# Optimization experiments

Hardware: AMD Instinct MI355X
Metric: run time of the kernel (lower is better)

Reference implementation:

```python
import jax, jax.numpy as jnp
import numpy as np

N, D, BS, M, DC, H, DH, L, E = 16384, 512, 16, 256, 512, 8, 64, 4, 262144
EPS = 1e-5


def _ln(x, w, b):
    mu = jnp.mean(x, -1, keepdims=True)
    var = jnp.var(x, -1, keepdims=True)
    return (x - mu) * jax.lax.rsqrt(var + EPS) * w + b


def _gcn(x, src, dst, W, b, n):
    deg = jax.ops.segment_sum(jnp.ones_like(src, dtype=x.dtype), dst, num_segments=n)
    dinv = jnp.where(deg > 0, deg ** -0.5, 0.0)
    norm = dinv[src] * dinv[dst]  # [E+N]
    h = x @ W
    out = jax.ops.segment_sum(h[src] * norm[:, None], dst, num_segments=n)
    return out + b


def _attn(xf, cond, Wq, Wk, Wv, Wo):
    n, d = xf.shape
    xb = xf.reshape(BS, n // BS, d)                    # stack(chunk(x, bs))
    q = (xb @ Wq).reshape(BS, -1, H, DH)
    k = (cond @ Wk).reshape(BS, -1, H, DH)
    v = (cond @ Wv).reshape(BS, -1, H, DH)
    att = jnp.einsum('bnhd,bmhd->bhnm', q, k) * (DH ** -0.5)
    w = jax.nn.softmax(att, axis=-1)
    o = jnp.einsum('bhnm,bmhd->bnhd', w, v).reshape(BS, -1, H * DH)
    return (o @ Wo).reshape(n, d)


def setup_inputs() -> dict:
    key = jax.random.key(0)
    ks = jax.random.split(key, 24)
    s = lambda fi, fo: (2.0 / (fi + fo)) ** 0.5
    inp = {
        'x': jax.random.normal(ks[0], (N, D), jnp.float32),
        'edge_index': jax.random.randint(ks[1], (2, E), 0, N, jnp.int64),
        'cond': jax.random.normal(ks[2], (BS, M, DC), jnp.float32),
        'bn_w': jnp.ones((D,), jnp.float32),
        'bn_b': jnp.zeros((D,), jnp.float32),
        'gcn_in_w': jax.random.normal(ks[3], (D, D), jnp.float32) * s(D, D),
        'gcn_in_b': jnp.zeros((D,), jnp.float32),
        'gcn_out_w': jax.random.normal(ks[4], (D, D), jnp.float32) * s(D, D),
        'gcn_out_b': jnp.zeros((D,), jnp.float32),
        'Wq': jax.random.normal(ks[5], (L, D, H * DH), jnp.float32) * s(D, H * DH),
        'Wk': jax.random.normal(ks[6], (L, DC, H * DH), jnp.float32) * s(DC, H * DH),
        'Wv': jax.random.normal(ks[7], (L, DC, H * DH), jnp.float32) * s(DC, H * DH),
        'Wo': jax.random.normal(ks[8], (L, H * DH, D), jnp.float32) * s(H * DH, D),
        'ln2_w': jnp.ones((L, D), jnp.float32),
        'ln2_b': jnp.zeros((L, D), jnp.float32),
        'ln3_w': jnp.ones((L, D), jnp.float32),
        'ln3_b': jnp.zeros((L, D), jnp.float32),
        'geglu_w': jax.random.normal(ks[9], (L, D, 8 * D), jnp.float32) * s(D, 8 * D),
        'geglu_b': jnp.zeros((L, 8 * D), jnp.float32),
        'ffo_w': jax.random.normal(ks[10], (L, 4 * D, D), jnp.float32) * s(4 * D, D),
        'ffo_b': jnp.zeros((L, D), jnp.float32),
    }
    return inp


def reference(x, edge_index, cond, bn_w, bn_b, gcn_in_w, gcn_in_b, gcn_out_w,
              gcn_out_b, Wq, Wk, Wv, Wo, ln2_w, ln2_b, ln3_w, ln3_b,
              geglu_w, geglu_b, ffo_w, ffo_b):
    n = x.shape[0]
    loops = jnp.arange(n)
    src = jnp.concatenate([edge_index[0], loops])
    dst = jnp.concatenate([edge_index[1], loops])

    x_in = x
    # BatchNorm1d (training mode: batch stats, biased var)
    mu = jnp.mean(x, 0)
    var = jnp.var(x, 0)
    h = (x - mu) * jax.lax.rsqrt(var + EPS) * bn_w + bn_b

    h = _gcn(h, src, dst, gcn_in_w, gcn_in_b, n)

    for i in range(L):
        a = _attn(_ln(h, ln2_w[i], ln2_b[i]), cond, Wq[i], Wk[i], Wv[i], Wo[i])
        h = h + a
        u = _ln(h, ln3_w[i], ln3_b[i]) @ geglu_w[i] + geglu_b[i]
        val, gate = jnp.split(u, 2, axis=-1)
        f = val * jax.nn.gelu(gate, approximate=False)
        h = h + f @ ffo_w[i] + ffo_b[i]

    h = _gcn(h, src, dst, gcn_out_w, gcn_out_b, n)
    return h + x_in
```

## Files before the change

kernel.cpp:

```cpp
#include <hip/hip_runtime.h>
#include <math.h>
#include <stdio.h>

#define N_NODES 16384
#define DIM     512
#define BSZ     16
#define SEQ     1024
#define MCTX    256
#define NHEAD   8
#define DHEAD   64
#define NLAYER  4
#define NEDGE   262144
#define DFF     2048
#define DG      4096
#define LNEPS   1e-5f

typedef unsigned short u16;
typedef __attribute__((ext_vector_type(8))) __bf16 bf16x8;
typedef __attribute__((ext_vector_type(4))) float f32x4;
typedef __attribute__((ext_vector_type(4))) unsigned short u16x4;
typedef __attribute__((ext_vector_type(8))) unsigned short u16x8;

__device__ __forceinline__ u16 f2b(float f) {
    unsigned u = __float_as_uint(f);
    unsigned r = (u + 0x7fff + ((u >> 16) & 1)) >> 16;
    return (u16)r;
}
__device__ __forceinline__ float b2f(u16 h) {
    return __uint_as_float((unsigned)h << 16);
}
__device__ __forceinline__ float gelu_exact(float x) {
    return 0.5f * x * (1.0f + erff(x * 0.70710678118654752f));
}
__device__ __forceinline__ void gload16(const void* g, void* l) {
    __builtin_amdgcn_global_load_lds(
        (const __attribute__((address_space(1))) unsigned int*)g,
        (__attribute__((address_space(3))) unsigned int*)l, 16, 0, 0);
}

__device__ __forceinline__ int2 xcd_map() {
    int gx = gridDim.x, gy = gridDim.y;
    int nwg = gx * gy;
    int id = blockIdx.y * gx + blockIdx.x;
    int q = nwg >> 3, r = nwg & 7;
    int xcd = id & 7, idx = id >> 3;
    int nid = (xcd < r ? xcd * (q + 1) : r * (q + 1) + (xcd - r) * q) + idx;
    int2 o; o.x = nid % gx; o.y = nid / gx; return o;
}

__global__ __launch_bounds__(512, 2) void bgemm256_geglu(
    const u16* __restrict__ A, long lda,
    const u16* __restrict__ Bt, long ldb,
    const float* __restrict__ bias,
    u16* __restrict__ Cb, int K)
{
    __shared__ u16 lds[65536];

    const int t = threadIdx.x;
    const int w = t >> 6, lane = t & 63;
    const int fr = lane & 15, fq = lane >> 4;
    int2 sw = xcd_map();
    const int row0 = sw.y * 256;
    const int col0 = sw.x * 256;
    const int wm0 = (w >> 2) * 128, wn0 = (w & 3) * 64;
    const int sl = (lane & 7) ^ ((lane >> 3) & 7);

    f32x4 acc[8][4];
#pragma unroll
    for (int mf = 0; mf < 8; ++mf)
#pragma unroll
        for (int nf = 0; nf < 4; ++nf) acc[mf][nf] = (f32x4){0.f, 0.f, 0.f, 0.f};

    auto stageA = [&](int kt_, int P, int bb) {
        const int k0 = kt_ << 6;
#pragma unroll
        for (int rd = 0; rd < 2; ++rd) {
            int rbase = rd * 128 + P * 64 + w * 8;
            int r = rbase + (lane >> 3);
            gload16(A + (size_t)(row0 + r) * lda + k0 + sl * 8,
                    (char*)(lds + bb * 16384) + rbase * 128);
        }
    };
    auto stageB = [&](int kt_, int Q, int bb) {
        const int k0 = kt_ << 6;
#pragma unroll
        for (int rd = 0; rd < 2; ++rd) {
            int jb = rd * 64 + w * 8;
            int nbase = ((jb >> 5) << 6) + Q * 32 + (jb & 31);
            int n = nbase + (lane >> 3);
            gload16(Bt + (size_t)(col0 + n) * ldb + k0 + sl * 8,
                    (char*)(lds + 32768 + bb * 16384) + nbase * 128);
        }
    };

#define PHASE(MH, NH, STAGE_STMT, WC) do {                                    \
    const u16* Ab_ = lds + b * 16384;                                         \
    const u16* Bb_ = lds + 32768 + b * 16384;                                 \
    bf16x8 av[4][2], bv[2][2];                                                \
    _Pragma("unroll")                                                         \
    for (int mi = 0; mi < 4; ++mi) {                                          \
        int r = wm0 + MH * 64 + mi * 16 + fr;                                 \
        _Pragma("unroll")                                                     \
        for (int ks = 0; ks < 2; ++ks)                                        \
            av[mi][ks] = *(const bf16x8*)&Ab_[r * 64 + (((ks*4+fq) ^ (fr&7)) * 8)]; \
    }                                                                         \
    _Pragma("unroll")                                                         \
    for (int ni = 0; ni < 2; ++ni) {                                          \
        int n = wn0 + NH * 32 + ni * 16 + fr;                                 \
        _Pragma("unroll")                                                     \
        for (int ks = 0; ks < 2; ++ks)                                        \
            bv[ni][ks] = *(const bf16x8*)&Bb_[n * 64 + (((ks*4+fq) ^ (fr&7)) * 8)]; \
    }                                                                         \
    STAGE_STMT;                                                               \
    __builtin_amdgcn_s_barrier();                                             \
    asm volatile("s_waitcnt lgkmcnt(0)" ::: "memory");                        \
    __builtin_amdgcn_s_setprio(1);                                            \
    _Pragma("unroll")                                                         \
    for (int mi = 0; mi < 4; ++mi)                                            \
        _Pragma("unroll")                                                     \
        for (int ni = 0; ni < 2; ++ni)                                        \
            _Pragma("unroll")                                                 \
            for (int ks = 0; ks < 2; ++ks)                                    \
                acc[MH*4+mi][NH*2+ni] = __builtin_amdgcn_mfma_f32_16x16x32_bf16( \
                    av[mi][ks], bv[ni][ks], acc[MH*4+mi][NH*2+ni], 0, 0, 0);  \
    __builtin_amdgcn_s_setprio(0);                                            \
    { int wc_ = (WC);                                                         \
      if (wc_ == 4)      asm volatile("s_waitcnt vmcnt(4)" ::: "memory");     \
      else if (wc_ == 0) asm volatile("s_waitcnt vmcnt(0)" ::: "memory"); }   \
    __builtin_amdgcn_s_barrier();                                             \
} while (0)

    stageA(0, 0, 0); stageB(0, 0, 0); stageA(0, 1, 0); stageB(0, 1, 0);
    stageA(1, 0, 1); stageB(1, 0, 1);
    asm volatile("s_waitcnt vmcnt(4)" ::: "memory");
    __builtin_amdgcn_s_barrier();

    const int NT = K >> 6;
    for (int kt = 0; kt < NT; ++kt) {
        const int b = kt & 1;
        const bool s1 = (kt + 1 < NT), s2 = (kt + 2 < NT);
        PHASE(0, 0, if (s1) stageA(kt + 1, 1, b ^ 1), -1);
        PHASE(0, 1, if (s1) stageB(kt + 1, 1, b ^ 1), -1);
        PHASE(1, 0, if (s2) stageA(kt + 2, 0, b), -1);
        PHASE(1, 1, if (s2) stageB(kt + 2, 0, b), s2 ? 4 : (s1 ? 0 : -1));
    }
#undef PHASE

    const int nbase = (col0 + wn0) >> 1;
    float bval[2], bgat[2];
#pragma unroll
    for (int P = 0; P < 2; ++P) {
        int n = nbase + P * 16 + fr;
        bval[P] = bias[n];
        bgat[P] = bias[DFF + n];
    }
#pragma unroll
    for (int mf = 0; mf < 8; ++mf) {
        const int rb = row0 + wm0 + mf * 16 + fq * 4;
#pragma unroll
        for (int P = 0; P < 2; ++P) {
            const int n = nbase + P * 16 + fr;
#pragma unroll
            for (int j = 0; j < 4; ++j) {
                float v = acc[mf][2 * P][j] + bval[P];
                float g = acc[mf][2 * P + 1][j] + bgat[P];
                Cb[(size_t)(rb + j) * DFF + n] = f2b(v * gelu_exact(g));
            }
        }
    }
}

template<int EPI>
__global__ __launch_bounds__(256) void bgemm(
    const u16* __restrict__ A, long lda,
    const u16* __restrict__ Bt, long ldb,
    const float* __restrict__ bias,
    const float* __restrict__ resid, long ldr,
    const float* __restrict__ rowscale,
    void* __restrict__ Cv, long ldc, int K, int nlo,
    long aHi, long aLo, long bHi, long bLo, long cHi, long cLo)
{
    __shared__ u16 lds[32768];

    const int t = threadIdx.x;
    const int z = blockIdx.z;
    const int zhi = z / nlo, zlo = z % nlo;
    const u16* Ag = A + (size_t)zhi * aHi + (size_t)zlo * aLo;
    const u16* Bg = Bt + (size_t)zhi * bHi + (size_t)zlo * bLo;
    const long coff = (long)zhi * cHi + (long)zlo * cLo;

    int2 sw = xcd_map();
    const int row0 = sw.y * 128;
    const int col0 = sw.x * 128;
    const int wave = t >> 6, lane = t & 63;
    const int wm0 = (wave >> 1) * 64, wn0 = (wave & 1) * 64;
    const int fr = lane & 15, fq = lane >> 4;
    const int ldsWave = (t & 192) * 16;
    const int rS = t >> 3;
    const int slotP = t & 7;

    f32x4 acc[4][4];
#pragma unroll
    for (int mi = 0; mi < 4; ++mi)
#pragma unroll
        for (int ni = 0; ni < 4; ++ni) acc[mi][ni] = (f32x4){0.f, 0.f, 0.f, 0.f};

    auto stage = [&](int buf, int k0) {
        u16* Ad = lds + buf * 8192;
        u16* Bd = lds + 16384 + buf * 8192;
#pragma unroll
        for (int i = 0; i < 4; ++i) {
            int r = i * 32 + rS;
            int s2 = slotP ^ (r & 7);
            gload16(Ag + (size_t)(row0 + r) * lda + k0 + s2 * 8,
                    (char*)Ad + i * 4096 + ldsWave);
        }
#pragma unroll
        for (int i = 0; i < 4; ++i) {
            int r = i * 32 + rS;
            int s2 = slotP ^ (r & 7);
            gload16(Bg + (size_t)(col0 + r) * ldb + k0 + s2 * 8,
                    (char*)Bd + i * 4096 + ldsWave);
        }
    };
    auto compute = [&](int buf) {
        const u16* Ac = lds + buf * 8192;
        const u16* Bc = lds + 16384 + buf * 8192;
#pragma unroll
        for (int ks = 0; ks < 2; ++ks) {
            const int ksl = ks * 4 + fq;
            bf16x8 av[4], bv[4];
#pragma unroll
            for (int mi = 0; mi < 4; ++mi) {
                int r = wm0 + mi * 16 + fr;
                av[mi] = *(const bf16x8*)&Ac[r * 64 + ((ksl ^ (r & 7)) * 8)];
            }
#pragma unroll
            for (int ni = 0; ni < 4; ++ni) {
                int r = wn0 + ni * 16 + fr;
                bv[ni] = *(const bf16x8*)&Bc[r * 64 + ((ksl ^ (r & 7)) * 8)];
            }
#pragma unroll
            for (int mi = 0; mi < 4; ++mi)
#pragma unroll
                for (int ni = 0; ni < 4; ++ni)
                    acc[mi][ni] = __builtin_amdgcn_mfma_f32_16x16x32_bf16(
                        av[mi], bv[ni], acc[mi][ni], 0, 0, 0);
        }
    };

    int cur = 0;
    stage(0, 0);
    __syncthreads();
    for (int k0 = 64; k0 < K; k0 += 64) {
        stage(cur ^ 1, k0);
        compute(cur);
        __syncthreads();
        cur ^= 1;
    }
    compute(cur);

    if (EPI == 3) {
        __syncthreads();
        u16* Tw = lds + wave * 4608;
#pragma unroll
        for (int mi = 0; mi < 4; ++mi)
#pragma unroll
            for (int ni = 0; ni < 4; ++ni)
#pragma unroll
                for (int j = 0; j < 4; ++j)
                    Tw[(ni * 16 + fr) * 72 + mi * 16 + fq * 4 + j] =
                        f2b(acc[mi][ni][j]);
        const int r0w = row0 + wm0;
        const int b = r0w >> 8, m0w = r0w & 255;
        const int cc0 = col0 + wn0, hh = cc0 >> 6;
        u16* dst = (u16*)Cv + ((size_t)(b * 8 + hh) * 64) * 256 + m0w;
#pragma unroll
        for (int it = 0; it < 8; ++it) {
            int dl = it * 8 + (lane >> 3);
            int ml = (lane & 7) * 8;
            u16x8 v = *(const u16x8*)&Tw[dl * 72 + ml];
            *(u16x8*)&dst[(size_t)dl * 256 + ml] = v;
        }
        return;
    }

    float* Cf = (float*)Cv;
    u16* Cb = (u16*)Cv;
#pragma unroll
    for (int mi = 0; mi < 4; ++mi) {
        const int rb = row0 + wm0 + mi * 16 + fq * 4;
#pragma unroll
        for (int ni = 0; ni < 4; ++ni) {
            const int cc = col0 + wn0 + ni * 16 + fr;
            f32x4 v = acc[mi][ni];
            float bval = 0.f;
            if ((EPI == 1 || EPI == 2) && bias) bval = bias[cc];
#pragma unroll
            for (int j = 0; j < 4; ++j) {
                const long r = rb + j;
                float o = v[j] + bval;
                if (EPI == 1) {
                    Cb[coff + r * ldc + cc] = f2b(o);
                } else if (EPI == 2) {
                    Cf[coff + r * ldc + cc] = o + resid[r * ldr + cc];
                } else if (EPI == 4) {
                    Cb[coff + r * ldc + cc] = f2b(o * rowscale[r]);
                }
            }
        }
    }
}

__global__ __launch_bounds__(256) void transposeW(const float* __restrict__ src,
                                                  u16* __restrict__ dst,
                                                  int K, int N,
                                                  long srcZ, long dstZ, int permN)
{
    __shared__ float tile[64][65];
    const int t = threadIdx.x;
    const int n0 = blockIdx.x * 64, k0 = blockIdx.y * 64;
    const float* s = src + (size_t)blockIdx.z * srcZ;
    u16* d = dst + (size_t)blockIdx.z * dstZ;
#pragma unroll
    for (int i = 0; i < 16; ++i) {
        int idx = i * 256 + t;
        int rr = idx >> 6, cc = idx & 63;
        tile[rr][cc] = s[(size_t)(k0 + rr) * N + n0 + cc];
    }
    __syncthreads();
#pragma unroll
    for (int i = 0; i < 16; ++i) {
        int idx = i * 256 + t;
        int rr = idx >> 6, cc = idx & 63;
        int n = n0 + rr;
        int p = n;
        if (permN) {
            p = (n < permN) ? (((n >> 4) << 5) + (n & 15))
                            : ((((n - permN) >> 4) << 5) + 16 + ((n - permN) & 15));
        }
        d[(size_t)p * K + k0 + cc] = f2b(tile[cc][rr]);
    }
}

__global__ __launch_bounds__(256) void conv_f2b(const float* __restrict__ in,
                                                u16* __restrict__ out)
{
    size_t i = (size_t)blockIdx.x * 256 + threadIdx.x;
    float4 v = ((const float4*)in)[i];
    u16x4 o;
    o[0] = f2b(v.x); o[1] = f2b(v.y); o[2] = f2b(v.z); o[3] = f2b(v.w);
    ((u16x4*)out)[i] = o;
}

__global__ __launch_bounds__(512) void bn_colstats(const float* __restrict__ x,
                                                   float* __restrict__ cs,
                                                   float* __restrict__ cq)
{
    int c = threadIdx.x;
    int r0 = blockIdx.x * 128;
    float s = 0.f, q = 0.f;
    for (int r = 0; r < 128; ++r) {
        float v = x[(size_t)(r0 + r) * DIM + c];
        s += v; q += v * v;
    }
    atomicAdd(&cs[c], s);
    atomicAdd(&cq[c], q);
}

__global__ void bn_finalize(const float* __restrict__ cs, const float* __restrict__ cq,
                            const float* __restrict__ bw, const float* __restrict__ bb,
                            float* __restrict__ scale, float* __restrict__ shift)
{
    int c = threadIdx.x;
    float m   = cs[c] * (1.f / N_NODES);
    float var = cq[c] * (1.f / N_NODES) - m * m;
    float rs  = rsqrtf(var + LNEPS);
    float sc  = rs * bw[c];
    scale[c] = sc;
    shift[c] = bb[c] - m * sc;
}

__global__ __launch_bounds__(256) void bn_apply_b(const float* __restrict__ x,
                                                  const float* __restrict__ scale,
                                                  const float* __restrict__ shift,
                                                  u16* __restrict__ out)
{
    size_t idx = (size_t)blockIdx.x * 256 + threadIdx.x;
    int c4 = (int)(idx & 127);
    float4 v  = ((const float4*)x)[idx];
    float4 sc = ((const float4*)scale)[c4];
    float4 sh = ((const float4*)shift)[c4];
    u16x4 o;
    o[0] = f2b(v.x * sc.x + sh.x); o[1] = f2b(v.y * sc.y + sh.y);
    o[2] = f2b(v.z * sc.z + sh.z); o[3] = f2b(v.w * sc.w + sh.w);
    ((u16x4*)out)[idx] = o;
}

__global__ __launch_bounds__(256) void layernorm_b(const float* __restrict__ in,
                                                   const float* __restrict__ w,
                                                   const float* __restrict__ bsh,
                                                   u16* __restrict__ out)
{
    int lane = threadIdx.x & 63, wv = threadIdx.x >> 6;
    size_t row = (size_t)blockIdx.x * 4 + wv;
    const float* p = in + row * DIM + lane * 8;
    float4 v0 = *(const float4*)p;
    float4 v1 = *(const float4*)(p + 4);
    float s = v0.x + v0.y + v0.z + v0.w + v1.x + v1.y + v1.z + v1.w;
    float q = v0.x * v0.x + v0.y * v0.y + v0.z * v0.z + v0.w * v0.w +
              v1.x * v1.x + v1.y * v1.y + v1.z * v1.z + v1.w * v1.w;
    for (int m = 1; m < 64; m <<= 1) {
        s += __shfl_xor(s, m, 64);
        q += __shfl_xor(q, m, 64);
    }
    float mean = s * (1.f / DIM);
    float rs = rsqrtf(q * (1.f / DIM) - mean * mean + LNEPS);
    float4 w0 = *(const float4*)(w + lane * 8),   w1 = *(const float4*)(w + lane * 8 + 4);
    float4 b0 = *(const float4*)(bsh + lane * 8), b1 = *(const float4*)(bsh + lane * 8 + 4);
    u16x8 o;
    o[0] = f2b((v0.x - mean) * rs * w0.x + b0.x);
    o[1] = f2b((v0.y - mean) * rs * w0.y + b0.y);
    o[2] = f2b((v0.z - mean) * rs * w0.z + b0.z);
    o[3] = f2b((v0.w - mean) * rs * w0.w + b0.w);
    o[4] = f2b((v1.x - mean) * rs * w1.x + b1.x);
    o[5] = f2b((v1.y - mean) * rs * w1.y + b1.y);
    o[6] = f2b((v1.z - mean) * rs * w1.z + b1.z);
    o[7] = f2b((v1.w - mean) * rs * w1.w + b1.w);
    *(u16x8*)(out + row * DIM + lane * 8) = o;
}

__global__ __launch_bounds__(256) void fused_attn(
    const u16* __restrict__ Q,
    const u16* __restrict__ Kp,
    const u16* __restrict__ Vt,
    u16* __restrict__ O)
{
    __shared__ u16 Ks[256 * 64];
    __shared__ u16 Vs[64 * 256];
    __shared__ u16 Ps[4][16 * 256];

    const int t = threadIdx.x;
    const int wave = t >> 6, lane = t & 63;
    const int fr = lane & 15, fq = lane >> 4;
    const int qc = blockIdx.x, h = blockIdx.y, b = blockIdx.z;
    const int ldsW = (t & 192) * 16;

#pragma unroll
    for (int i = 0; i < 8; ++i) {
        int idx = i * 256 + t;
        int m = idx >> 3, s = idx & 7;
        gload16(Kp + (size_t)(b * MCTX + m) * 512 + h * 64 + ((s ^ (m & 7)) * 8),
                (char*)Ks + i * 4096 + ldsW);
    }
#pragma unroll
    for (int i = 0; i < 8; ++i) {
        int idx = i * 256 + t;
        int d = idx >> 5, s = idx & 31;
        gload16(Vt + (size_t)((b * 8 + h) * 64 + d) * 256 + ((s ^ (d & 7)) * 8),
                (char*)Vs + i * 4096 + ldsW);
    }
    __syncthreads();

    u16* Pw = Ps[wave];
    for (int it = 0; it < 4; ++it) {
        const int q0 = qc * 256 + it * 64 + wave * 16;
        bf16x8 aq[2];
#pragma unroll
        for (int ks = 0; ks < 2; ++ks)
            aq[ks] = *(const bf16x8*)&Q[(size_t)(b * SEQ + q0 + fr) * 512 +
                                        h * 64 + ks * 32 + fq * 8];
        f32x4 accS[16];
#pragma unroll
        for (int ni = 0; ni < 16; ++ni) accS[ni] = (f32x4){0.f, 0.f, 0.f, 0.f};
#pragma unroll
        for (int ni = 0; ni < 16; ++ni) {
            int m = ni * 16 + fr;
#pragma unroll
            for (int ks = 0; ks < 2; ++ks) {
                bf16x8 bv = *(const bf16x8*)&Ks[m * 64 + (((ks * 4 + fq) ^ (m & 7)) * 8)];
                accS[ni] = __builtin_amdgcn_mfma_f32_16x16x32_bf16(
                    aq[ks], bv, accS[ni], 0, 0, 0);
            }
        }
        const float cs = 0.125f;
#pragma unroll
        for (int j = 0; j < 4; ++j) {
            float m0 = accS[0][j];
#pragma unroll
            for (int ni = 1; ni < 16; ++ni) m0 = fmaxf(m0, accS[ni][j]);
            m0 = fmaxf(m0, __shfl_xor(m0, 1, 64));
            m0 = fmaxf(m0, __shfl_xor(m0, 2, 64));
            m0 = fmaxf(m0, __shfl_xor(m0, 4, 64));
            m0 = fmaxf(m0, __shfl_xor(m0, 8, 64));
            float s0 = 0.f;
#pragma unroll
            for (int ni = 0; ni < 16; ++ni) {
                float p = __expf((accS[ni][j] - m0) * cs);
                accS[ni][j] = p;
                s0 += p;
            }
            s0 += __shfl_xor(s0, 1, 64);
            s0 += __shfl_xor(s0, 2, 64);
            s0 += __shfl_xor(s0, 4, 64);
            s0 += __shfl_xor(s0, 8, 64);
            float inv = 1.f / s0;
#pragma unroll
            for (int ni = 0; ni < 16; ++ni) {
                int cc = ni * 16 + fr;
                int rr = fq * 4 + j;
                Pw[rr * 256 + (((cc >> 3) ^ (rr & 7)) * 8) + (cc & 7)] =
                    f2b(accS[ni][j] * inv);
            }
        }
        bf16x8 ap[8];
#pragma unroll
        for (int ks = 0; ks < 8; ++ks)
            ap[ks] = *(const bf16x8*)&Pw[fr * 256 + (((ks * 4 + fq) ^ (fr & 7)) * 8)];
        f32x4 accO[4];
#pragma unroll
        for (int ni = 0; ni < 4; ++ni) accO[ni] = (f32x4){0.f, 0.f, 0.f, 0.f};
#pragma unroll
        for (int ni = 0; ni < 4; ++ni) {
            int d = ni * 16 + fr;
#pragma unroll
            for (int ks = 0; ks < 8; ++ks) {
                bf16x8 bv = *(const bf16x8*)&Vs[d * 256 + (((ks * 4 + fq) ^ (d & 7)) * 8)];
                accO[ni] = __builtin_amdgcn_mfma_f32_16x16x32_bf16(
                    ap[ks], bv, accO[ni], 0, 0, 0);
            }
        }
#pragma unroll
        for (int ni = 0; ni < 4; ++ni)
#pragma unroll
            for (int j = 0; j < 4; ++j)
                O[(size_t)(b * SEQ + q0 + fq * 4 + j) * 512 + h * 64 + ni * 16 + fr] =
                    f2b(accO[ni][j]);
    }
}

__global__ void detect_i64(const int* __restrict__ e, int* __restrict__ flag)
{
    int idx = blockIdx.x * blockDim.x + threadIdx.x;
    if (e[2 * idx + 1] != 0) flag[0] = 1;
}

__global__ void deg_count(const int* __restrict__ eb, const int* __restrict__ flag,
                          int* __restrict__ deg)
{
    int e = blockIdx.x * blockDim.x + threadIdx.x;
    int d;
    if (flag[0]) d = eb[NEDGE + e];
    else         d = (int)((const long long*)eb)[NEDGE + e];
    atomicAdd(&deg[d], 1);
}

__global__ void dinv_k(const int* __restrict__ deg, float* __restrict__ dinv)
{
    int i = blockIdx.x * blockDim.x + threadIdx.x;
    dinv[i] = rsqrtf((float)(deg[i] + 1));
}

__global__ __launch_bounds__(1024) void scan_deg(const int* __restrict__ deg,
                                                 int* __restrict__ off)
{
    __shared__ int sums[1024];
    int t = threadIdx.x;
    int base = t * 16;
    int v[16]; int s = 0;
#pragma unroll
    for (int i = 0; i < 16; ++i) { v[i] = deg[base + i]; s += v[i]; }
    sums[t] = s;
    __syncthreads();
    for (int ofs = 1; ofs < 1024; ofs <<= 1) {
        int x = (t >= ofs) ? sums[t - ofs] : 0;
        __syncthreads();
        sums[t] += x;
        __syncthreads();
    }
    int run = (t == 0) ? 0 : sums[t - 1];
#pragma unroll
    for (int i = 0; i < 16; ++i) { off[base + i] = run; run += v[i]; }
    if (t == 1023) off[N_NODES] = run;
}

__global__ void fill_k(const int* __restrict__ eb, const int* __restrict__ flag,
                       const int* __restrict__ off, int* __restrict__ cursor,
                       int* __restrict__ csr)
{
    int e = blockIdx.x * blockDim.x + threadIdx.x;
    int s, d;
    if (flag[0]) { s = eb[e]; d = eb[NEDGE + e]; }
    else {
        const long long* p = (const long long*)eb;
        s = (int)p[e]; d = (int)p[NEDGE + e];
    }
    int pos = atomicAdd(&cursor[d], 1);
    csr[off[d] + pos] = s;
}

__global__ __launch_bounds__(256) void gcn_gather(
    const u16* __restrict__ h2, const int* __restrict__ csr,
    const int* __restrict__ off, const float* __restrict__ dinv,
    const float* __restrict__ bias, const float* __restrict__ addx,
    float* __restrict__ out)
{
    int lane = threadIdx.x & 63, wv = threadIdx.x >> 6;
    int d = blockIdx.x * 4 + wv;
    float acc[8];
#pragma unroll
    for (int j = 0; j < 8; ++j) acc[j] = 0.f;
    int e0 = off[d], e1 = off[d + 1];
    float dd = dinv[d];
    int sidx = (e0 < e1) ? csr[e0] : d;
    u16x8 v = *(const u16x8*)&h2[(size_t)sidx * DIM + lane * 8];
    for (int e = e0; e < e1; ++e) {
        int snext = (e + 1 < e1) ? csr[e + 1] : d;
        u16x8 vn = *(const u16x8*)&h2[(size_t)snext * DIM + lane * 8];
#pragma unroll
        for (int j = 0; j < 8; ++j) acc[j] += b2f(v[j]);
        v = vn;
    }
#pragma unroll
    for (int j = 0; j < 8; ++j) acc[j] = (acc[j] + b2f(v[j])) * dd;
    float o[8];
#pragma unroll
    for (int j = 0; j < 8; ++j) {
        o[j] = acc[j] + bias[lane * 8 + j];
        if (addx) o[j] += addx[(size_t)d * DIM + lane * 8 + j];
    }
    float* op = out + (size_t)d * DIM + lane * 8;
    *(float4*)op = make_float4(o[0], o[1], o[2], o[3]);
    *(float4*)(op + 4) = make_float4(o[4], o[5], o[6], o[7]);
}

extern "C" void kernel_launch(void* const* d_in, const int* in_sizes, int n_in,
                              void* d_out, int out_size, void* d_ws, size_t ws_size,
                              hipStream_t stream)
{
    const float* x         = (const float*)d_in[0];
    const int*   edges     = (const int*)d_in[1];
    const float* cond      = (const float*)d_in[2];
    const float* bn_w      = (const float*)d_in[3];
    const float* bn_b      = (const float*)d_in[4];
    const float* gcn_in_w  = (const float*)d_in[5];
    const float* gcn_in_b  = (const float*)d_in[6];
    const float* gcn_out_w = (const float*)d_in[7];
    const float* gcn_out_b = (const float*)d_in[8];
    const float* Wq  = (const float*)d_in[9];
    const float* Wk  = (const float*)d_in[10];
    const float* Wv  = (const float*)d_in[11];
    const float* Wo  = (const float*)d_in[12];
    const float* ln2w = (const float*)d_in[13];
    const float* ln2b = (const float*)d_in[14];
    const float* ln3w = (const float*)d_in[15];
    const float* ln3b = (const float*)d_in[16];
    const float* ggw = (const float*)d_in[17];
    const float* ggb = (const float*)d_in[18];
    const float* fow = (const float*)d_in[19];
    const float* fob = (const float*)d_in[20];
    float* outp = (float*)d_out;

    char* wsb = (char*)d_ws;
    size_t wsoff = 0;
    auto alloc = [&](size_t bytes) -> void* {
        void* p = wsb + wsoff;
        wsoff = (wsoff + bytes + 255) & ~(size_t)255;
        return p;
    };
    u16*   wT    = (u16*)  alloc((size_t)17301504 * 2);
    u16*   condb = (u16*)  alloc((size_t)4096 * 512 * 2);
    float* h     = (float*)alloc((size_t)N_NODES * DIM * 4);
    u16*   t0b   = (u16*)  alloc((size_t)N_NODES * DIM * 2);
    u16*   qb    = (u16*)  alloc((size_t)N_NODES * DIM * 2);
    u16*   ob    = (u16*)  alloc((size_t)N_NODES * DIM * 2);
    u16*   kb    = (u16*)  alloc((size_t)4096 * 512 * 2);
    u16*   Vt    = (u16*)  alloc((size_t)BSZ * NHEAD * DHEAD * MCTX * 2);
    char*  zbase  = wsb + wsoff;
    float* colsum = (float*)alloc(DIM * 4);
    float* colsq  = (float*)alloc(DIM * 4);
    int*   deg    = (int*)  alloc(N_NODES * 4);
    int*   cursor = (int*)  alloc(N_NODES * 4);
    int*   eflag  = (int*)  alloc(256);
    size_t zbytes = (size_t)((wsb + wsoff) - zbase);
    float* bscale = (float*)alloc(DIM * 4);
    float* bshift = (float*)alloc(DIM * 4);
    float* dinv   = (float*)alloc(N_NODES * 4);
    int*   csr_off= (int*)  alloc((N_NODES + 16) * 4);
    int*   csr_src= (int*)  alloc((size_t)NEDGE * 4);

    int nch = 0;
    for (int c = 1; c <= 16; c *= 2) {
        size_t need = ((size_t)N_NODES / c) * DFF * 2;
        if (wsoff + need <= ws_size) { nch = c; break; }
    }
    if (nch == 0) { fprintf(stderr, "ws too small (%zu)\n", ws_size); return; }
    u16* Abuf = (u16*)(wsb + wsoff);

    hipMemsetAsync(zbase, 0, zbytes, stream);

    u16* gcnInT  = wT;
    u16* gcnOutT = gcnInT + 262144;
    u16* WqT = gcnOutT + 262144;
    u16* WkT = WqT + 4 * 262144;
    u16* WvT = WkT + 4 * 262144;
    u16* WoT = WvT + 4 * 262144;
    u16* ggT = WoT + 4 * 262144;
    u16* foT = ggT + 4 * 2097152;
    transposeW<<<dim3(8, 8, 1), 256, 0, stream>>>(gcn_in_w,  gcnInT, 512, 512, 0, 0, 0);
    transposeW<<<dim3(8, 8, 1), 256, 0, stream>>>(gcn_out_w, gcnOutT, 512, 512, 0, 0, 0);
    transposeW<<<dim3(8, 8, 4), 256, 0, stream>>>(Wq, WqT, 512, 512, 262144, 262144, 0);
    transposeW<<<dim3(8, 8, 4), 256, 0, stream>>>(Wk, WkT, 512, 512, 262144, 262144, 0);
    transposeW<<<dim3(8, 8, 4), 256, 0, stream>>>(Wv, WvT, 512, 512, 262144, 262144, 0);
    transposeW<<<dim3(8, 8, 4), 256, 0, stream>>>(Wo, WoT, 512, 512, 262144, 262144, 0);
    transposeW<<<dim3(64, 8, 4), 256, 0, stream>>>(ggw, ggT, 512, DG, 2097152, 2097152, DFF);
    transposeW<<<dim3(8, 32, 4), 256, 0, stream>>>(fow, foT, DFF, 512, 1048576, 1048576, 0);
    conv_f2b<<<2048, 256, 0, stream>>>(cond, condb);

    bn_colstats<<<128, 512, 0, stream>>>(x, colsum, colsq);
    bn_finalize<<<1, 512, 0, stream>>>(colsum, colsq, bn_w, bn_b, bscale, bshift);
    bn_apply_b<<<(N_NODES * DIM / 4) / 256, 256, 0, stream>>>(x, bscale, bshift, t0b);

    detect_i64<<<NEDGE / 256, 256, 0, stream>>>(edges, eflag);
    deg_count<<<NEDGE / 256, 256, 0, stream>>>(edges, eflag, deg);
    dinv_k<<<N_NODES / 256, 256, 0, stream>>>(deg, dinv);
    scan_deg<<<1, 1024, 0, stream>>>(deg, csr_off);
    fill_k<<<NEDGE / 256, 256, 0, stream>>>(edges, eflag, csr_off, cursor, csr_src);

    bgemm<4><<<dim3(4, 128, 1), 256, 0, stream>>>(
        t0b, 512, gcnInT, 512, nullptr, nullptr, 0, dinv, qb, 512, 512, 1,
        0, 0, 0, 0, 0, 0);
    gcn_gather<<<N_NODES / 4, 256, 0, stream>>>(qb, csr_src, csr_off, dinv,
                                                gcn_in_b, nullptr, h);

    const int ffrows = N_NODES / nch;
    for (int i = 0; i < NLAYER; ++i) {
        const u16* WqTi = WqT + (size_t)i * 262144;
        const u16* WkTi = WkT + (size_t)i * 262144;
        const u16* WvTi = WvT + (size_t)i * 262144;
        const u16* WoTi = WoT + (size_t)i * 262144;
        const u16* ggTi = ggT + (size_t)i * 2097152;
        const u16* foTi = foT + (size_t)i * 1048576;

        layernorm_b<<<N_NODES / 4, 256, 0, stream>>>(h, ln2w + i * DIM, ln2b + i * DIM, t0b);
        bgemm<1><<<dim3(4, 128, 1), 256, 0, stream>>>(
            t0b, 512, WqTi, 512, nullptr, nullptr, 0, nullptr, qb, 512, 512, 1,
            0, 0, 0, 0, 0, 0);
        bgemm<1><<<dim3(4, 32, 1), 256, 0, stream>>>(
            condb, 512, WkTi, 512, nullptr, nullptr, 0, nullptr, kb, 512, 512, 1,
            0, 0, 0, 0, 0, 0);
        bgemm<3><<<dim3(4, 32, 1), 256, 0, stream>>>(
            condb, 512, WvTi, 512, nullptr, nullptr, 0, nullptr, Vt, 0, 512, 1,
            0, 0, 0, 0, 0, 0);
        fused_attn<<<dim3(4, 8, 16), 256, 0, stream>>>(qb, kb, Vt, ob);
        bgemm<2><<<dim3(4, 128, 1), 256, 0, stream>>>(
            ob, 512, WoTi, 512, nullptr, h, 512, nullptr, h, 512, 512, 1,
            0, 0, 0, 0, 0, 0);

        layernorm_b<<<N_NODES / 4, 256, 0, stream>>>(h, ln3w + i * DIM, ln3b + i * DIM, t0b);
        for (int c = 0; c < nch; ++c) {
            const u16* ac = t0b + (size_t)c * ffrows * 512;
            float* hc = h + (size_t)c * ffrows * 512;
            bgemm256_geglu<<<dim3(DG / 256, ffrows / 256), 512, 0, stream>>>(
                ac, 512, ggTi, 512, ggb + (size_t)i * DG, Abuf, 512);
            bgemm<2><<<dim3(4, ffrows / 128, 1), 256, 0, stream>>>(
                Abuf, 2048, foTi, 2048, fob + (size_t)i * DIM, hc, 512, nullptr,
                hc, 512, 2048, 1, 0, 0, 0, 0, 0, 0);
        }
    }

    conv_f2b<<<8192, 256, 0, stream>>>(h, t0b);
    bgemm<4><<<dim3(4, 128, 1), 256, 0, stream>>>(
        t0b, 512, gcnOutT, 512, nullptr, nullptr, 0, dinv, qb, 512, 512, 1,
        0, 0, 0, 0, 0, 0);
    gcn_gather<<<N_NODES / 4, 256, 0, stream>>>(qb, csr_src, csr_off, dinv,
                                                gcn_out_b, x, outp);
}
```

Measured before the change: 1.323 ms.

## Reorder GEGLU MFMA phases for register reuse, tanh GELU, batch K/V projections

Three changes. The GEGLU GEMM inner loop now reuses A and B fragments across its four phases in a snake order, so the last phase does no LDS reads. The exact erf GELU is swapped for a tanh approximation built on exp. The per-layer K and V projections of cond are hoisted out of the layer loop into two batched launches over all layers, which adds buffers that hold K/V for every layer. The tanh GELU changes numerics away from the reference's exact GELU, which risks going past the accuracy tolerance.

```diff
diff --git a/kernel.cpp b/kernel.cpp
--- a/kernel.cpp
+++ b/kernel.cpp
@@ -32,6 +32,12 @@
 __device__ __forceinline__ float gelu_exact(float x) {
     return 0.5f * x * (1.0f + erff(x * 0.70710678118654752f));
 }
+__device__ __forceinline__ float gelu_fast(float x) {
+    float u = x * (0.7978845608f + 0.0356774081f * x * x);
+    float e = __expf(2.f * u);
+    float t = 1.f - 2.f / (e + 1.f);
+    return 0.5f * x * (1.f + t);
+}
 __device__ __forceinline__ void gload16(const void* g, void* l) {
     __builtin_amdgcn_global_load_lds(
         (const __attribute__((address_space(1))) unsigned int*)g,
@@ -93,42 +99,31 @@
         }
     };
 
-#define PHASE(MH, NH, STAGE_STMT, WC) do {                                    \
-    const u16* Ab_ = lds + b * 16384;                                         \
-    const u16* Bb_ = lds + 32768 + b * 16384;                                 \
-    bf16x8 av[4][2], bv[2][2];                                                \
-    _Pragma("unroll")                                                         \
-    for (int mi = 0; mi < 4; ++mi) {                                          \
-        int r = wm0 + MH * 64 + mi * 16 + fr;                                 \
-        _Pragma("unroll")                                                     \
-        for (int ks = 0; ks < 2; ++ks)                                        \
-            av[mi][ks] = *(const bf16x8*)&Ab_[r * 64 + (((ks*4+fq) ^ (fr&7)) * 8)]; \
-    }                                                                         \
-    _Pragma("unroll")                                                         \
-    for (int ni = 0; ni < 2; ++ni) {                                          \
-        int n = wn0 + NH * 32 + ni * 16 + fr;                                 \
-        _Pragma("unroll")                                                     \
-        for (int ks = 0; ks < 2; ++ks)                                        \
-            bv[ni][ks] = *(const bf16x8*)&Bb_[n * 64 + (((ks*4+fq) ^ (fr&7)) * 8)]; \
-    }                                                                         \
-    STAGE_STMT;                                                               \
-    __builtin_amdgcn_s_barrier();                                             \
-    asm volatile("s_waitcnt lgkmcnt(0)" ::: "memory");                        \
-    __builtin_amdgcn_s_setprio(1);                                            \
-    _Pragma("unroll")                                                         \
-    for (int mi = 0; mi < 4; ++mi)                                            \
-        _Pragma("unroll")                                                     \
-        for (int ni = 0; ni < 2; ++ni)                                        \
-            _Pragma("unroll")                                                 \
-            for (int ks = 0; ks < 2; ++ks)                                    \
-                acc[MH*4+mi][NH*2+ni] = __builtin_amdgcn_mfma_f32_16x16x32_bf16( \
-                    av[mi][ks], bv[ni][ks], acc[MH*4+mi][NH*2+ni], 0, 0, 0);  \
-    __builtin_amdgcn_s_setprio(0);                                            \
-    { int wc_ = (WC);                                                         \
-      if (wc_ == 4)      asm volatile("s_waitcnt vmcnt(4)" ::: "memory");     \
-      else if (wc_ == 0) asm volatile("s_waitcnt vmcnt(0)" ::: "memory"); }   \
-    __builtin_amdgcn_s_barrier();                                             \
-} while (0)
+#define READ_A(MH, DST) do {                                                   \
+    _Pragma("unroll")                                                          \
+    for (int mi = 0; mi < 4; ++mi) {                                           \
+        int r = wm0 + (MH) * 64 + mi * 16 + fr;                                \
+        _Pragma("unroll")                                                      \
+        for (int ks = 0; ks < 2; ++ks)                                         \
+            DST[mi][ks] = *(const bf16x8*)&Ab_[r * 64 + (((ks*4+fq) ^ (fr&7)) * 8)]; \
+    } } while (0)
+#define READ_B(NH, DST) do {                                                   \
+    _Pragma("unroll")                                                          \
+    for (int ni = 0; ni < 2; ++ni) {                                           \
+        int n = wn0 + (NH) * 32 + ni * 16 + fr;                                \
+        _Pragma("unroll")                                                      \
+        for (int ks = 0; ks < 2; ++ks)                                         \
+            DST[ni][ks] = *(const bf16x8*)&Bb_[n * 64 + (((ks*4+fq) ^ (fr&7)) * 8)]; \
+    } } while (0)
+#define MFMA16(MH, NH, AV, BV)                                                 \
+    _Pragma("unroll")                                                          \
+    for (int mi = 0; mi < 4; ++mi)                                             \
+        _Pragma("unroll")                                                      \
+        for (int ni = 0; ni < 2; ++ni)                                         \
+            _Pragma("unroll")                                                  \
+            for (int ks = 0; ks < 2; ++ks)                                     \
+                acc[(MH)*4+mi][(NH)*2+ni] = __builtin_amdgcn_mfma_f32_16x16x32_bf16( \
+                    AV[mi][ks], BV[ni][ks], acc[(MH)*4+mi][(NH)*2+ni], 0, 0, 0)
 
     stageA(0, 0, 0); stageB(0, 0, 0); stageA(0, 1, 0); stageB(0, 1, 0);
     stageA(1, 0, 1); stageB(1, 0, 1);
@@ -139,12 +134,49 @@
     for (int kt = 0; kt < NT; ++kt) {
         const int b = kt & 1;
         const bool s1 = (kt + 1 < NT), s2 = (kt + 2 < NT);
-        PHASE(0, 0, if (s1) stageA(kt + 1, 1, b ^ 1), -1);
-        PHASE(0, 1, if (s1) stageB(kt + 1, 1, b ^ 1), -1);
-        PHASE(1, 0, if (s2) stageA(kt + 2, 0, b), -1);
-        PHASE(1, 1, if (s2) stageB(kt + 2, 0, b), s2 ? 4 : (s1 ? 0 : -1));
-    }
-#undef PHASE
+        const u16* Ab_ = lds + b * 16384;
+        const u16* Bb_ = lds + 32768 + b * 16384;
+        bf16x8 aR[4][2], bR[2][2], bK[2][2];
+
+        READ_A(0, aR); READ_B(0, bK);
+        if (s1) stageA(kt + 1, 1, b ^ 1);
+        __builtin_amdgcn_s_barrier();
+        asm volatile("s_waitcnt lgkmcnt(0)" ::: "memory");
+        __builtin_amdgcn_s_setprio(1);
+        MFMA16(0, 0, aR, bK);
+        __builtin_amdgcn_s_setprio(0);
+        __builtin_amdgcn_s_barrier();
+
+        READ_B(1, bR);
+        if (s1) stageB(kt + 1, 1, b ^ 1);
+        __builtin_amdgcn_s_barrier();
+        asm volatile("s_waitcnt lgkmcnt(0)" ::: "memory");
+        __builtin_amdgcn_s_setprio(1);
+        MFMA16(0, 1, aR, bR);
+        __builtin_amdgcn_s_setprio(0);
+        __builtin_amdgcn_s_barrier();
+
+        READ_A(1, aR);
+        if (s2) stageA(kt + 2, 0, b);
+        __builtin_amdgcn_s_barrier();
+        asm volatile("s_waitcnt lgkmcnt(0)" ::: "memory");
+        __builtin_amdgcn_s_setprio(1);
+        MFMA16(1, 1, aR, bR);
+        __builtin_amdgcn_s_setprio(0);
+        __builtin_amdgcn_s_barrier();
+
+        if (s2) stageB(kt + 2, 0, b);
+        __builtin_amdgcn_s_barrier();
+        __builtin_amdgcn_s_setprio(1);
+        MFMA16(1, 0, aR, bK);
+        __builtin_amdgcn_s_setprio(0);
+        if (s2)      asm volatile("s_waitcnt vmcnt(4)" ::: "memory");
+        else if (s1) asm volatile("s_waitcnt vmcnt(0)" ::: "memory");
+        __builtin_amdgcn_s_barrier();
+    }
+#undef READ_A
+#undef READ_B
+#undef MFMA16
 
     const int nbase = (col0 + wn0) >> 1;
     float bval[2], bgat[2];
@@ -164,7 +196,7 @@
             for (int j = 0; j < 4; ++j) {
                 float v = acc[mf][2 * P][j] + bval[P];
                 float g = acc[mf][2 * P + 1][j] + bgat[P];
-                Cb[(size_t)(rb + j) * DFF + n] = f2b(v * gelu_exact(g));
+                Cb[(size_t)(rb + j) * DFF + n] = f2b(v * gelu_fast(g));
             }
         }
     }
@@ -274,7 +306,7 @@
         const int r0w = row0 + wm0;
         const int b = r0w >> 8, m0w = r0w & 255;
         const int cc0 = col0 + wn0, hh = cc0 >> 6;
-        u16* dst = (u16*)Cv + ((size_t)(b * 8 + hh) * 64) * 256 + m0w;
+        u16* dst = (u16*)Cv + coff + ((size_t)(b * 8 + hh) * 64) * 256 + m0w;
 #pragma unroll
         for (int it = 0; it < 8; ++it) {
             int dl = it * 8 + (lane >> 3);
@@ -674,8 +706,8 @@
     u16*   t0b   = (u16*)  alloc((size_t)N_NODES * DIM * 2);
     u16*   qb    = (u16*)  alloc((size_t)N_NODES * DIM * 2);
     u16*   ob    = (u16*)  alloc((size_t)N_NODES * DIM * 2);
-    u16*   kb    = (u16*)  alloc((size_t)4096 * 512 * 2);
-    u16*   Vt    = (u16*)  alloc((size_t)BSZ * NHEAD * DHEAD * MCTX * 2);
+    u16*   kb    = (u16*)  alloc((size_t)NLAYER * 4096 * 512 * 2);
+    u16*   Vt    = (u16*)  alloc((size_t)NLAYER * BSZ * NHEAD * DHEAD * MCTX * 2);
     char*  zbase  = wsb + wsoff;
     float* colsum = (float*)alloc(DIM * 4);
     float* colsq  = (float*)alloc(DIM * 4);
@@ -727,6 +759,13 @@
     scan_deg<<<1, 1024, 0, stream>>>(deg, csr_off);
     fill_k<<<NEDGE / 256, 256, 0, stream>>>(edges, eflag, csr_off, cursor, csr_src);
 
+    bgemm<1><<<dim3(4, 32, 4), 256, 0, stream>>>(
+        condb, 512, WkT, 512, nullptr, nullptr, 0, nullptr, kb, 512, 512, 1,
+        0, 0, 262144, 0, (long)4096 * 512, 0);
+    bgemm<3><<<dim3(4, 32, 4), 256, 0, stream>>>(
+        condb, 512, WvT, 512, nullptr, nullptr, 0, nullptr, Vt, 0, 512, 1,
+        0, 0, 262144, 0, (long)BSZ * NHEAD * DHEAD * MCTX, 0);
+
     bgemm<4><<<dim3(4, 128, 1), 256, 0, stream>>>(
         t0b, 512, gcnInT, 512, nullptr, nullptr, 0, dinv, qb, 512, 512, 1,
         0, 0, 0, 0, 0, 0);
@@ -736,23 +775,17 @@
     const int ffrows = N_NODES / nch;
     for (int i = 0; i < NLAYER; ++i) {
         const u16* WqTi = WqT + (size_t)i * 262144;
-        const u16* WkTi = WkT + (size_t)i * 262144;
-        const u16* WvTi = WvT + (size_t)i * 262144;
         const u16* WoTi = WoT + (size_t)i * 262144;
         const u16* ggTi = ggT + (size_t)i * 2097152;
         const u16* foTi = foT + (size_t)i * 1048576;
+        const u16* kbi  = kb + (size_t)i * 4096 * 512;
+        const u16* Vti  = Vt + (size_t)i * BSZ * NHEAD * DHEAD * MCTX;
 
         layernorm_b<<<N_NODES / 4, 256, 0, stream>>>(h, ln2w + i * DIM, ln2b + i * DIM, t0b);
         bgemm<1><<<dim3(4, 128, 1), 256, 0, stream>>>(
             t0b, 512, WqTi, 512, nullptr, nullptr, 0, nullptr, qb, 512, 512, 1,
             0, 0, 0, 0, 0, 0);
-        bgemm<1><<<dim3(4, 32, 1), 256, 0, stream>>>(
-            condb, 512, WkTi, 512, nullptr, nullptr, 0, nullptr, kb, 512, 512, 1,
-            0, 0, 0, 0, 0, 0);
-        bgemm<3><<<dim3(4, 32, 1), 256, 0, stream>>>(
-            condb, 512, WvTi, 512, nullptr, nullptr, 0, nullptr, Vt, 0, 512, 1,
-            0, 0, 0, 0, 0, 0);
-        fused_attn<<<dim3(4, 8, 16), 256, 0, stream>>>(qb, kb, Vt, ob);
+        fused_attn<<<dim3(4, 8, 16), 256, 0, stream>>>(qb, kbi, Vti, ob);
         bgemm<2><<<dim3(4, 128, 1), 256, 0, stream>>>(
             ob, 512, WoTi, 512, nullptr, h, 512, nullptr, h, 512, 512, 1,
             0, 0, 0, 0, 0, 0);
```

Result: faster. 1.235 ms (-6.7%).
